# Kernel tuning notes

Measured on AMD Instinct MI355X. Metric: run time of the kernel, lower is better.

The kernel has to match this reference:

```python
import jax, jax.numpy as jnp
import numpy as np

B, S, H, NH = 4, 4096, 1024, 16
HD = H // NH  # head_dim = 64


def setup_inputs() -> dict:
    key = jax.random.key(0)
    ks = jax.random.split(key, 8)
    scale = 0.02
    return {
        "hidden_states": jax.random.normal(ks[0], (B, S, H), dtype=jnp.float32),
        "attention_mask": jnp.ones((B, S), dtype=jnp.float32),
        "Wq": jax.random.normal(ks[1], (H, H), dtype=jnp.float32) * scale,
        "bq": jnp.zeros((H,), dtype=jnp.float32),
        "Wk": jax.random.normal(ks[2], (H, H), dtype=jnp.float32) * scale,
        "bk": jnp.zeros((H,), dtype=jnp.float32),
        "Wv": jax.random.normal(ks[3], (H, H), dtype=jnp.float32) * scale,
        "bv": jnp.zeros((H,), dtype=jnp.float32),
        "Wo": jax.random.normal(ks[4], (H, H), dtype=jnp.float32) * scale,
        "bo": jnp.zeros((H,), dtype=jnp.float32),
    }


def _heads(x):
    # [B,S,H] -> [B,NH,S,HD]
    b, s, _ = x.shape
    return x.reshape(b, s, NH, HD).transpose(0, 2, 1, 3)


def reference(hidden_states, attention_mask, Wq, bq, Wk, bk, Wv, bv, Wo, bo):
    b, s, _ = hidden_states.shape
    q = _heads(hidden_states @ Wq.T + bq)
    k = _heads(hidden_states @ Wk.T + bk)
    v = _heads(hidden_states @ Wv.T + bv)

    m = attention_mask[:, None, :, None]  # [B,1,S,1]
    k = k * m
    v = v * m

    # Faithful to the torch code: kv_i = matmul(k_i[b,h,1,d], v_i[b,h,d,1])
    # is the SCALAR dot product k_t . v_t, broadcast-added to the [d,d] state.
    # => state_t = (cumsum_t k_t.v_t) * ones(d,d)
    # => o_t = state_t @ q_t = (cumsum_t k_t.v_t) * sum_j q_t[j], same for every i.
    dots = jnp.einsum('bhsd,bhsd->bhs', k, v)        # scalar k.v per step
    cum = jnp.cumsum(dots, axis=-1)                  # running state scalar
    qsum = jnp.sum(q, axis=-1)                       # [B,NH,S]
    o = jnp.broadcast_to((cum * qsum)[..., None], q.shape)  # [B,NH,S,HD]

    out = o.transpose(0, 2, 1, 3).reshape(b, s, NH * HD)
    out = out @ Wo.T + bo  # dropout is identity (eval / p handled as 0)

    # final state: last cumulative scalar broadcast over the [d,d] matrix
    state = jnp.broadcast_to(cum[:, :, -1, None, None], (b, NH, HD, HD))
    return out, state
```

## Files before the change

### kernel.cpp

```cpp
#include <hip/hip_runtime.h>
#include <hip/hip_bf16.h>


typedef __attribute__((ext_vector_type(4))) float f32x4;
typedef __attribute__((ext_vector_type(8))) short bf16x8;
typedef __attribute__((ext_vector_type(8))) unsigned short u16x8;
typedef unsigned int u32;

#define GLDS16(g, l)                                                            \
  __builtin_amdgcn_global_load_lds((const __attribute__((address_space(1))) u32*)(g), \
                                   (__attribute__((address_space(3))) u32*)(l), 16, 0, 0)
#define MFMA16(a, b, c) __builtin_amdgcn_mfma_f32_16x16x32_bf16(a, b, c, 0, 0, 0)
#define LGK0 do { asm volatile("s_waitcnt lgkmcnt(0)" ::: "memory"); \
                  __builtin_amdgcn_sched_barrier(0); } while (0)

__device__ __forceinline__ unsigned short f2bf(float f) {
  union { float f; u32 u; } x; x.f = f;
  u32 r = (x.u + 0x7fffu + ((x.u >> 16) & 1u)) >> 16;
  return (unsigned short)r;
}

__device__ __forceinline__ bf16x8 pack8(const f32x4& lo, const f32x4& hi) {
  union { bf16x8 v; u32 w[4]; } r;
  union { __hip_bfloat162 h; u32 u; } c;
  c.h = __float22bfloat162_rn(make_float2(lo.x, lo.y)); r.w[0] = c.u;
  c.h = __float22bfloat162_rn(make_float2(lo.z, lo.w)); r.w[1] = c.u;
  c.h = __float22bfloat162_rn(make_float2(hi.x, hi.y)); r.w[2] = c.u;
  c.h = __float22bfloat162_rn(make_float2(hi.z, hi.w)); r.w[3] = c.u;
  return r.v;
}

__global__ void k_prep(const float* __restrict__ Wq, const float* __restrict__ bq,
                       const float* __restrict__ Wk, const float* __restrict__ bk,
                       const float* __restrict__ Wv, const float* __restrict__ bv,
                       const float* __restrict__ Wo,
                       unsigned short* __restrict__ Wkb, unsigned short* __restrict__ Wvb,
                       unsigned short* __restrict__ SWb, float* __restrict__ WosT,
                       float* __restrict__ scal) {
  int blk = blockIdx.x, t = threadIdx.x;
  if (blk < 2048) {
    const float* src = (blk < 1024) ? Wk : Wv;
    unsigned short* dst = (blk < 1024) ? Wkb : Wvb;
    size_t i = ((size_t)(blk & 1023) * 256 + t) * 4;
    f32x4 v = *(const f32x4*)(src + i);
    dst[i + 0] = f2bf(v.x); dst[i + 1] = f2bf(v.y);
    dst[i + 2] = f2bf(v.z); dst[i + 3] = f2bf(v.w);
  } else {
    int b2 = blk - 2048;
    if (b2 < 128) {
      int o = b2 * 256 + t;
      int r = o >> 10, c = o & 1023;
      float s = 0.f;
      if (r < 16) {
        for (int d = 0; d < 64; ++d) s += Wq[(size_t)(r * 64 + d) * 1024 + c];
      } else {
        int h = r - 16;
        for (int d = 0; d < 64; ++d) {
          int j = h * 64 + d;
          s += bv[j] * Wk[(size_t)j * 1024 + c] + bk[j] * Wv[(size_t)j * 1024 + c];
        }
      }
      SWb[o] = f2bf(s);
    } else if (b2 < 192) {
      int o = (b2 - 128) * 256 + t;
      int h = o >> 10, j = o & 1023;
      float s = 0.f;
      for (int d = 0; d < 64; ++d) s += Wo[(size_t)j * 1024 + h * 64 + d];
      WosT[o] = s;
    } else {
      if (t < 16) {
        float s = 0.f;
        for (int d = 0; d < 64; ++d) s += bq[t * 64 + d];
        scal[t] = s;
      } else if (t < 32) {
        int h = t - 16;
        float s = 0.f;
        for (int d = 0; d < 64; ++d) s += bk[h * 64 + d] * bv[h * 64 + d];
        scal[t] = s;
      }
    }
  }
}

#define NT 32
#define BUFS 17408
__global__ __launch_bounds__(512, 2) void k_dualgemm(
    const float* __restrict__ X,
    const unsigned short* __restrict__ Wkb,
    const unsigned short* __restrict__ Wvb,
    const unsigned short* __restrict__ SWb,
    float* __restrict__ dotsT, float* __restrict__ qsumT, float* __restrict__ dotbT) {
  extern __shared__ __align__(16) unsigned short lds[];
  int orig = blockIdx.x;
  int wg = (orig & 7) * 64 + (orig >> 3);
  int bx = wg & 7, by = wg >> 3;
  int row0 = by << 8, col0 = bx << 7;
  int tid = threadIdx.x, wid = tid >> 6, lane = tid & 63;
  int wrM = wid >> 1, wcN = wid & 1;
  int fr = lane & 15, fg = lane >> 4;
  bool side = (bx == 0);
  bool swv = side && (wid < 2);

  int rA = tid >> 2, sA = tid & 3;
  int gA = sA ^ ((tid >> 3) & 3);
  const float* pA0 = X + (size_t)(row0 + rA) * 1024 + gA * 8;
  const float* pA1 = pA0 + (size_t)128 * 1024;
  int wo0 = rA * 32 + sA * 8;
  int wo1 = wo0 + 4096;

  int rB = tid >> 2;
  int uswB = (((tid & 3) ^ ((tid >> 3) & 3)) << 3);
  const unsigned short* sK = Wkb + (size_t)(col0 + rB) * 1024 + uswB;
  const unsigned short* sV = Wvb + (size_t)(col0 + rB) * 1024 + uswB;
  const unsigned short* sS = SWb + (size_t)(tid >> 2) * 1024 + uswB;
  int dK = 8192 + (wid << 9), dV = 12288 + (wid << 9), dS = 16384 + (wid << 9);

  int ubo = (fg ^ ((fr >> 1) & 3)) << 3;
  int aro = (wrM * 64 + fr) * 32 + ubo;
  int bro = (wcN * 64 + fr) * 32 + ubo;
  int swo = 16384 + (wcN * 16 + fr) * 32 + ubo;

  f32x4 ck[4][4] = {{0}}, cv[4][4] = {{0}};
  f32x4 qa[4] = {0, 0, 0, 0};

  {
    f32x4 xl0 = *(const f32x4*)(pA0);     f32x4 xh0 = *(const f32x4*)(pA0 + 4);
    f32x4 xl1 = *(const f32x4*)(pA1);     f32x4 xh1 = *(const f32x4*)(pA1 + 4);
#pragma unroll
    for (int p = 0; p < 3; ++p) {
      int ko = p << 5;
      GLDS16(sK + ko, lds + p * BUFS + dK);
      GLDS16(sV + ko, lds + p * BUFS + dV);
      if (swv) GLDS16(sS + ko, lds + p * BUFS + dS);
    }
    if (swv) { asm volatile("s_waitcnt vmcnt(6)" ::: "memory"); }
    else     { asm volatile("s_waitcnt vmcnt(4)" ::: "memory"); }
    *(bf16x8*)(lds + wo0) = pack8(xl0, xh0);
    *(bf16x8*)(lds + wo1) = pack8(xl1, xh1);
    asm volatile("s_waitcnt lgkmcnt(0)" ::: "memory");
    __builtin_amdgcn_s_barrier();
  }

  for (int t = 0; t < NT; ++t) {
    const int rb = (t & 3) * BUFS;
    const bool st1 = (t + 1 < NT);
    const bool st3 = (t + 3 < NT);
    const int ko1 = (t + 1) << 5;
    const int ko3 = (t + 3) << 5;
    const int wb3 = ((t + 3) & 3) * BUFS;

    bf16x8 a[4], bk[4];
#pragma unroll
    for (int mi = 0; mi < 4; ++mi) a[mi] = *(const bf16x8*)(lds + rb + aro + mi * 512);
#pragma unroll
    for (int ni = 0; ni < 4; ++ni) bk[ni] = *(const bf16x8*)(lds + rb + 8192 + bro + ni * 512);
    f32x4 xl0, xh0, xl1, xh1;
    if (st1) {
      xl0 = *(const f32x4*)(pA0 + ko1); xh0 = *(const f32x4*)(pA0 + ko1 + 4);
      xl1 = *(const f32x4*)(pA1 + ko1); xh1 = *(const f32x4*)(pA1 + ko1 + 4);
    }
    LGK0;
    __builtin_amdgcn_s_setprio(1);
#pragma unroll
    for (int mi = 0; mi < 4; ++mi)
#pragma unroll
      for (int ni = 0; ni < 4; ++ni)
        ck[mi][ni] = MFMA16(a[mi], bk[ni], ck[mi][ni]);
    __builtin_amdgcn_s_setprio(0);

    bf16x8 bv[4], sw;
#pragma unroll
    for (int ni = 0; ni < 4; ++ni) bv[ni] = *(const bf16x8*)(lds + rb + 12288 + bro + ni * 512);
    if (side) sw = *(const bf16x8*)(lds + rb + swo);
    if (st3) {
      GLDS16(sK + ko3, lds + wb3 + dK);
      GLDS16(sV + ko3, lds + wb3 + dV);
      if (swv) GLDS16(sS + ko3, lds + wb3 + dS);
    }
    LGK0;
    __builtin_amdgcn_s_setprio(1);
#pragma unroll
    for (int mi = 0; mi < 4; ++mi)
#pragma unroll
      for (int ni = 0; ni < 4; ++ni)
        cv[mi][ni] = MFMA16(a[mi], bv[ni], cv[mi][ni]);
    if (side) {
#pragma unroll
      for (int mi = 0; mi < 4; ++mi) qa[mi] = MFMA16(a[mi], sw, qa[mi]);
    }
    __builtin_amdgcn_s_setprio(0);

    if (st1) {
      if (t < NT - 3) {
        if (swv) { asm volatile("s_waitcnt vmcnt(3)" ::: "memory"); }
        else     { asm volatile("s_waitcnt vmcnt(2)" ::: "memory"); }
      } else {
        asm volatile("s_waitcnt vmcnt(0)" ::: "memory");
      }
      unsigned short* Aw = lds + ((t + 1) & 3) * BUFS;
      *(bf16x8*)(Aw + wo0) = pack8(xl0, xh0);
      *(bf16x8*)(Aw + wo1) = pack8(xl1, xh1);
      asm volatile("s_waitcnt lgkmcnt(0)" ::: "memory");
    } else {
      asm volatile("s_waitcnt vmcnt(0)" ::: "memory");
    }
    __builtin_amdgcn_s_barrier();
  }

  float part[4][4];
#pragma unroll
  for (int mi = 0; mi < 4; ++mi)
#pragma unroll
    for (int q = 0; q < 4; ++q) {
      float s = 0.f;
#pragma unroll
      for (int ni = 0; ni < 4; ++ni) s += ck[mi][ni][q] * cv[mi][ni][q];
      part[mi][q] = s;
    }
#pragma unroll
  for (int r = 0; r < 4; ++r) {
#pragma unroll
    for (int mi = 0; mi < 4; ++mi)
#pragma unroll
      for (int q = 0; q < 4; ++q)
        part[mi][q] += __shfl_xor(part[mi][q], 1 << r, 64);
  }
  int h = bx * 2 + wcN;
  if (fr == 0) {
#pragma unroll
    for (int mi = 0; mi < 4; ++mi)
#pragma unroll
      for (int q = 0; q < 4; ++q)
        dotsT[(size_t)h * 16384 + row0 + wrM * 64 + mi * 16 + fg * 4 + q] = part[mi][q];
  }
  if (side) {
    float* dst = (wcN == 0) ? qsumT : dotbT;
#pragma unroll
    for (int mi = 0; mi < 4; ++mi)
#pragma unroll
      for (int q = 0; q < 4; ++q)
        dst[(size_t)fr * 16384 + row0 + wrM * 64 + mi * 16 + fg * 4 + q] = qa[mi][q];
  }
}

__global__ void k_cumsum(const float* __restrict__ dotsT, const float* __restrict__ dotbT,
                         const float* __restrict__ qsumT, const float* __restrict__ scal,
                         const float* __restrict__ mask,
                         float* __restrict__ coef, float* __restrict__ state) {
  __shared__ float csum[256];
  int b = blockIdx.x >> 4, h = blockIdx.x & 15;
  int t = threadIdx.x;
  float bqs = scal[h], dbc = scal[16 + h];
  size_t m0 = (size_t)b * 4096;
  const float* dro = dotsT + (size_t)h * 16384 + m0;
  const float* dbo = dotbT + (size_t)h * 16384 + m0;
  const float* qso = qsumT + (size_t)h * 16384 + m0;
  const float* mko = mask + m0;
  float loc[16], run = 0.f;
  int s0 = t * 16;
#pragma unroll
  for (int i = 0; i < 16; ++i) {
    int ii = s0 + i;
    float mk = mko[ii];
    float d = (dro[ii] + dbo[ii] + dbc) * mk * mk;
    run += d;
    loc[i] = run;
  }
  csum[t] = run;
  __syncthreads();
  for (int off = 1; off < 256; off <<= 1) {
    float v = (t >= off) ? csum[t - off] : 0.f;
    __syncthreads();
    csum[t] += v;
    __syncthreads();
  }
  float prefix = csum[t] - run;
#pragma unroll
  for (int i = 0; i < 16; ++i) {
    int ii = s0 + i;
    float cum = prefix + loc[i];
    coef[(m0 + ii) * 16 + h] = cum * (qso[ii] + bqs);
  }
  float total = csum[255];
  float* sp = state + (size_t)(b * 16 + h) * 4096;
  for (int i = t; i < 4096; i += 256) sp[i] = total;
}

__global__ __launch_bounds__(256) void k_outgemm(const float* __restrict__ coef,
                                                 const float* __restrict__ WosT,
                                                 const float* __restrict__ bo,
                                                 float* __restrict__ out) {
  int t = threadIdx.x;
  int j0 = t * 4;
  f32x4 w4[16];
#pragma unroll
  for (int hh = 0; hh < 16; ++hh) w4[hh] = *(const f32x4*)&WosT[hh * 1024 + j0];
  f32x4 bov = *(const f32x4*)&bo[j0];
  size_t m0 = (size_t)blockIdx.x * 32;
  for (int mi = 0; mi < 32; ++mi) {
    size_t m = m0 + mi;
    const float* cm = &coef[m * 16];
    f32x4 acc = bov;
#pragma unroll
    for (int hh = 0; hh < 16; ++hh) acc += w4[hh] * cm[hh];
    *(f32x4*)&out[m * 1024 + j0] = acc;
  }
}

extern "C" void kernel_launch(void* const* d_in, const int* in_sizes, int n_in,
                              void* d_out, int out_size, void* d_ws, size_t ws_size,
                              hipStream_t stream) {
  const float* X    = (const float*)d_in[0];
  const float* mask = (const float*)d_in[1];
  const float* Wq   = (const float*)d_in[2];
  const float* bq   = (const float*)d_in[3];
  const float* Wk   = (const float*)d_in[4];
  const float* bk   = (const float*)d_in[5];
  const float* Wv   = (const float*)d_in[6];
  const float* bv   = (const float*)d_in[7];
  const float* Wo   = (const float*)d_in[8];
  const float* bo   = (const float*)d_in[9];
  float* out   = (float*)d_out;
  float* state = out + (size_t)16384 * 1024;

  char* w = (char*)d_ws;
  unsigned short* Wkb = (unsigned short*)w; w += (size_t)1024 * 1024 * 2;
  unsigned short* Wvb = (unsigned short*)w; w += (size_t)1024 * 1024 * 2;
  unsigned short* SWb = (unsigned short*)w; w += (size_t)32 * 1024 * 2;
  float* WosT  = (float*)w; w += (size_t)16 * 1024 * 4;
  float* scal  = (float*)w; w += 256;
  float* dotsT = (float*)w; w += (size_t)16 * 16384 * 4;
  float* qsumT = (float*)w; w += (size_t)16 * 16384 * 4;
  float* dotbT = (float*)w; w += (size_t)16 * 16384 * 4;
  float* coef  = (float*)w; w += (size_t)16384 * 16 * 4;

  (void)hipFuncSetAttribute((const void*)k_dualgemm,
                            hipFuncAttributeMaxDynamicSharedMemorySize, 139264);

  hipLaunchKernelGGL(k_prep,     dim3(2241), dim3(256), 0, stream,
                     Wq, bq, Wk, bk, Wv, bv, Wo, Wkb, Wvb, SWb, WosT, scal);
  hipLaunchKernelGGL(k_dualgemm, dim3(512),  dim3(512), 139264, stream, X, Wkb, Wvb, SWb,
                     dotsT, qsumT, dotbT);
  hipLaunchKernelGGL(k_cumsum,   dim3(64),   dim3(256), 0, stream, dotsT, dotbT, qsumT, scal,
                     mask, coef, state);
  hipLaunchKernelGGL(k_outgemm,  dim3(512),  dim3(256), 0, stream, coef, WosT, bo, out);
}
```

Baseline: 110.3 us.

## Load A operand fragments directly from global into registers, bypassing LDS

Each wave now loads its own X rows straight from global memory into registers, in the MFMA fragment layout, and packs them to bf16 in registers instead of staging the A tile through LDS. This removes the LDS write/read of A and one barrier path. It also shrinks the per-stage LDS buffer so the kernel needs about half the shared memory. In exchange, the two waves that share a row block both fetch the same X rows, doubling global/L2 reads of X, and register pressure rises from the staging arrays.

```diff
diff --git a/kernel.cpp b/kernel.cpp
--- a/kernel.cpp
+++ b/kernel.cpp
@@ -83,7 +83,7 @@
 }
 
 #define NT 32
-#define BUFS 17408
+#define BUFS 9216
 __global__ __launch_bounds__(512, 2) void k_dualgemm(
     const float* __restrict__ X,
     const unsigned short* __restrict__ Wkb,
@@ -101,45 +101,41 @@
   bool side = (bx == 0);
   bool swv = side && (wid < 2);
 
-  int rA = tid >> 2, sA = tid & 3;
-  int gA = sA ^ ((tid >> 3) & 3);
-  const float* pA0 = X + (size_t)(row0 + rA) * 1024 + gA * 8;
-  const float* pA1 = pA0 + (size_t)128 * 1024;
-  int wo0 = rA * 32 + sA * 8;
-  int wo1 = wo0 + 4096;
+  const float* pA[4];
+#pragma unroll
+  for (int mi = 0; mi < 4; ++mi)
+    pA[mi] = X + (size_t)(row0 + wrM * 64 + mi * 16 + fr) * 1024 + fg * 8;
 
   int rB = tid >> 2;
   int uswB = (((tid & 3) ^ ((tid >> 3) & 3)) << 3);
   const unsigned short* sK = Wkb + (size_t)(col0 + rB) * 1024 + uswB;
   const unsigned short* sV = Wvb + (size_t)(col0 + rB) * 1024 + uswB;
-  const unsigned short* sS = SWb + (size_t)(tid >> 2) * 1024 + uswB;
-  int dK = 8192 + (wid << 9), dV = 12288 + (wid << 9), dS = 16384 + (wid << 9);
+  const unsigned short* sS = SWb + (size_t)rB * 1024 + uswB;
+  int dK = wid << 9, dV = 4096 + (wid << 9), dS = 8192 + (wid << 9);
 
   int ubo = (fg ^ ((fr >> 1) & 3)) << 3;
-  int aro = (wrM * 64 + fr) * 32 + ubo;
   int bro = (wcN * 64 + fr) * 32 + ubo;
-  int swo = 16384 + (wcN * 16 + fr) * 32 + ubo;
+  int swo = 8192 + (wcN * 16 + fr) * 32 + ubo;
 
   f32x4 ck[4][4] = {{0}}, cv[4][4] = {{0}};
   f32x4 qa[4] = {0, 0, 0, 0};
-
-  {
-    f32x4 xl0 = *(const f32x4*)(pA0);     f32x4 xh0 = *(const f32x4*)(pA0 + 4);
-    f32x4 xl1 = *(const f32x4*)(pA1);     f32x4 xh1 = *(const f32x4*)(pA1 + 4);
-#pragma unroll
-    for (int p = 0; p < 3; ++p) {
-      int ko = p << 5;
-      GLDS16(sK + ko, lds + p * BUFS + dK);
-      GLDS16(sV + ko, lds + p * BUFS + dV);
-      if (swv) GLDS16(sS + ko, lds + p * BUFS + dS);
-    }
-    if (swv) { asm volatile("s_waitcnt vmcnt(6)" ::: "memory"); }
-    else     { asm volatile("s_waitcnt vmcnt(4)" ::: "memory"); }
-    *(bf16x8*)(lds + wo0) = pack8(xl0, xh0);
-    *(bf16x8*)(lds + wo1) = pack8(xl1, xh1);
-    asm volatile("s_waitcnt lgkmcnt(0)" ::: "memory");
-    __builtin_amdgcn_s_barrier();
-  }
+  f32x4 stgL[4], stgH[4];
+
+#pragma unroll
+  for (int mi = 0; mi < 4; ++mi) {
+    stgL[mi] = *(const f32x4*)(pA[mi]);
+    stgH[mi] = *(const f32x4*)(pA[mi] + 4);
+  }
+#pragma unroll
+  for (int p = 0; p < 3; ++p) {
+    int ko = p << 5;
+    GLDS16(sK + ko, lds + p * BUFS + dK);
+    GLDS16(sV + ko, lds + p * BUFS + dV);
+    if (swv) GLDS16(sS + ko, lds + p * BUFS + dS);
+  }
+  if (swv) { asm volatile("s_waitcnt vmcnt(6)" ::: "memory"); }
+  else     { asm volatile("s_waitcnt vmcnt(4)" ::: "memory"); }
+  __builtin_amdgcn_s_barrier();
 
   for (int t = 0; t < NT; ++t) {
     const int rb = (t & 3) * BUFS;
@@ -151,32 +147,34 @@
 
     bf16x8 a[4], bk[4];
 #pragma unroll
-    for (int mi = 0; mi < 4; ++mi) a[mi] = *(const bf16x8*)(lds + rb + aro + mi * 512);
-#pragma unroll
-    for (int ni = 0; ni < 4; ++ni) bk[ni] = *(const bf16x8*)(lds + rb + 8192 + bro + ni * 512);
-    f32x4 xl0, xh0, xl1, xh1;
+    for (int mi = 0; mi < 4; ++mi) a[mi] = pack8(stgL[mi], stgH[mi]);
     if (st1) {
-      xl0 = *(const f32x4*)(pA0 + ko1); xh0 = *(const f32x4*)(pA0 + ko1 + 4);
-      xl1 = *(const f32x4*)(pA1 + ko1); xh1 = *(const f32x4*)(pA1 + ko1 + 4);
-    }
-    LGK0;
-    __builtin_amdgcn_s_setprio(1);
-#pragma unroll
-    for (int mi = 0; mi < 4; ++mi)
-#pragma unroll
-      for (int ni = 0; ni < 4; ++ni)
-        ck[mi][ni] = MFMA16(a[mi], bk[ni], ck[mi][ni]);
-    __builtin_amdgcn_s_setprio(0);
-
-    bf16x8 bv[4], sw;
-#pragma unroll
-    for (int ni = 0; ni < 4; ++ni) bv[ni] = *(const bf16x8*)(lds + rb + 12288 + bro + ni * 512);
-    if (side) sw = *(const bf16x8*)(lds + rb + swo);
+#pragma unroll
+      for (int mi = 0; mi < 4; ++mi) {
+        stgL[mi] = *(const f32x4*)(pA[mi] + ko1);
+        stgH[mi] = *(const f32x4*)(pA[mi] + ko1 + 4);
+      }
+    }
     if (st3) {
       GLDS16(sK + ko3, lds + wb3 + dK);
       GLDS16(sV + ko3, lds + wb3 + dV);
       if (swv) GLDS16(sS + ko3, lds + wb3 + dS);
     }
+#pragma unroll
+    for (int ni = 0; ni < 4; ++ni) bk[ni] = *(const bf16x8*)(lds + rb + bro + ni * 512);
+    LGK0;
+    __builtin_amdgcn_s_setprio(1);
+#pragma unroll
+    for (int mi = 0; mi < 4; ++mi)
+#pragma unroll
+      for (int ni = 0; ni < 4; ++ni)
+        ck[mi][ni] = MFMA16(a[mi], bk[ni], ck[mi][ni]);
+    __builtin_amdgcn_s_setprio(0);
+
+    bf16x8 bv[4], sw;
+#pragma unroll
+    for (int ni = 0; ni < 4; ++ni) bv[ni] = *(const bf16x8*)(lds + rb + 4096 + bro + ni * 512);
+    if (side) sw = *(const bf16x8*)(lds + rb + swo);
     LGK0;
     __builtin_amdgcn_s_setprio(1);
 #pragma unroll
@@ -191,20 +189,14 @@
     __builtin_amdgcn_s_setprio(0);
 
     if (st1) {
-      if (t < NT - 3) {
+      if (st3) {
         if (swv) { asm volatile("s_waitcnt vmcnt(3)" ::: "memory"); }
         else     { asm volatile("s_waitcnt vmcnt(2)" ::: "memory"); }
       } else {
         asm volatile("s_waitcnt vmcnt(0)" ::: "memory");
       }
-      unsigned short* Aw = lds + ((t + 1) & 3) * BUFS;
-      *(bf16x8*)(Aw + wo0) = pack8(xl0, xh0);
-      *(bf16x8*)(Aw + wo1) = pack8(xl1, xh1);
-      asm volatile("s_waitcnt lgkmcnt(0)" ::: "memory");
-    } else {
-      asm volatile("s_waitcnt vmcnt(0)" ::: "memory");
-    }
-    __builtin_amdgcn_s_barrier();
+      __builtin_amdgcn_s_barrier();
+    }
   }
 
   float part[4][4];
@@ -335,11 +327,11 @@
   float* coef  = (float*)w; w += (size_t)16384 * 16 * 4;
 
   (void)hipFuncSetAttribute((const void*)k_dualgemm,
-                            hipFuncAttributeMaxDynamicSharedMemorySize, 139264);
+                            hipFuncAttributeMaxDynamicSharedMemorySize, 73728);
 
   hipLaunchKernelGGL(k_prep,     dim3(2241), dim3(256), 0, stream,
                      Wq, bq, Wk, bk, Wv, bv, Wo, Wkb, Wvb, SWb, WosT, scal);
-  hipLaunchKernelGGL(k_dualgemm, dim3(512),  dim3(512), 139264, stream, X, Wkb, Wvb, SWb,
+  hipLaunchKernelGGL(k_dualgemm, dim3(512),  dim3(512), 73728, stream, X, Wkb, Wvb, SWb,
                      dotsT, qsumT, dotbT);
   hipLaunchKernelGGL(k_cumsum,   dim3(64),   dim3(256), 0, stream, dotsT, dotbT, qsumT, scal,
                      mask, coef, state);
```

New measurement: 217.2 us. 1.97x slower.
